# Optimization experiments

Hardware: AMD Instinct MI355X
Metric: run time of the kernel (lower is better)

## Reference

```python
import jax, jax.numpy as jnp
import numpy as np

N_NODES = 10000
N_EDGES = 160000
F_IN, D, DEPTH, F_OUT = 6, 512, 10, 1


def setup_inputs() -> dict:
    key = jax.random.key(0)
    ks = jax.random.split(key, 10)
    features = jax.random.normal(ks[0], (N_NODES, F_IN), dtype=jnp.float32)
    src = jax.random.randint(ks[1], (N_EDGES,), 0, N_NODES, dtype=jnp.int32)
    dst = jax.random.randint(ks[2], (N_EDGES,), 0, N_NODES, dtype=jnp.int32)
    s_in = 1.0 / np.sqrt(F_IN)
    s_h = 1.0 / np.sqrt(D)
    W_in = jax.random.uniform(ks[3], (F_IN, D), jnp.float32, -s_in, s_in)
    b_in = jax.random.uniform(ks[4], (D,), jnp.float32, -s_in, s_in)
    Ws = jax.random.uniform(ks[5], (DEPTH, D, D), jnp.float32, -s_h, s_h)
    bs = jax.random.uniform(ks[6], (DEPTH, D), jnp.float32, -s_h, s_h)
    W_out = jax.random.uniform(ks[7], (D, F_OUT), jnp.float32, -s_h, s_h)
    b_out = jax.random.uniform(ks[8], (F_OUT,), jnp.float32, -s_h, s_h)
    return {"features": features, "W_in": W_in, "b_in": b_in, "Ws": Ws,
            "bs": bs, "W_out": W_out, "b_out": b_out, "src": src, "dst": dst}


def reference(features, W_in, b_in, Ws, bs, W_out, b_out, src, dst):
    n = features.shape[0]
    # GCNLayer: aggregate = scatter-sum of neighbor features (copy_src + sum), then Linear
    agg = jax.ops.segment_sum(features[src], dst, num_segments=n)  # [N, F_in]
    x = jax.nn.relu(agg @ W_in + b_in)  # ReLU only after input layer (per forward)

    def step(x, wb):
        W, b = wb
        a = jax.ops.segment_sum(x[src], dst, num_segments=n)  # [N, D]
        return a @ W + b, None  # no activation between hidden GCN layers

    x, _ = jax.lax.scan(step, x, (Ws, bs))
    return x @ W_out + b_out  # [N, 1]
```

## Files before the change

### kernel.cpp

```cpp
#include <hip/hip_runtime.h>


#define N_NODES 10000
#define N_EDGES 160000
#define DEPTH   10

#define NB_G 40
#define NB_C 33
#define NB   (NB_G + NB_C)
#define BT   1024
#define NTHG (NB_G * BT)
#define NPB  250
#define ECAP 8192

__device__ __forceinline__ float ldA(const float* p) {
    return __hip_atomic_load(p, __ATOMIC_RELAXED, __HIP_MEMORY_SCOPE_AGENT);
}
__device__ __forceinline__ int ldAi(const int* p) {
    return __hip_atomic_load(p, __ATOMIC_RELAXED, __HIP_MEMORY_SCOPE_AGENT);
}
__device__ __forceinline__ void stA(float* p, float v) {
    __hip_atomic_store(p, v, __ATOMIC_RELAXED, __HIP_MEMORY_SCOPE_AGENT);
}
__device__ __forceinline__ void stAi(int* p, int v) {
    __hip_atomic_store(p, v, __ATOMIC_RELAXED, __HIP_MEMORY_SCOPE_AGENT);
}

__device__ __forceinline__ void group_bar(int* flags, int gi, int n, int target) {
    const int tx = threadIdx.x;
    asm volatile("s_waitcnt vmcnt(0)" ::: "memory");
    __syncthreads();
    if (tx == 0) stAi(&flags[gi * 32], target);
    if (tx < n && tx != gi) {
        while (ldAi(&flags[tx * 32]) < target) __builtin_amdgcn_s_sleep(1);
    }
    __syncthreads();
}

extern "C" __global__ void __launch_bounds__(BT, 1) gcn_mega(
    const float* __restrict__ features, const float* __restrict__ W_in,
    const float* __restrict__ b_in, const float* __restrict__ Ws,
    const float* __restrict__ bs, const float* __restrict__ W_out,
    const float* __restrict__ b_out, const int* __restrict__ src,
    const int* __restrict__ dst, float* __restrict__ out,
    int* g_arrive, int* c_arrive, int* rdv, int* deg, int* row_ptr,
    int* cursor, int* esrc, float* vbufs, float* gamma,
    float* rb0, float* rb1)
{
    __shared__ int   lds_e[ECAP];
    __shared__ float s_Wb[4096];
    __shared__ float s_vt[512];
    __shared__ float s_gam[16];
    __shared__ int   s_info[2];
    __shared__ int   s_wsum[16];

    const int tx = threadIdx.x;
    const int bx = blockIdx.x;

    if (bx >= NB_G) {
        const int gi   = bx - NB_G;
        const int cw   = gi * (BT / 64) + (tx >> 6);
        const int lane = tx & 63;
        for (int s = 0; s < DEPTH; s++) {
            const int l = 9 - s;
            if (cw <= 512) {
                float vin[8];
                if (s == 0) {
#pragma unroll
                    for (int c = 0; c < 8; c++) vin[c] = W_out[lane + 64 * c];
                } else {
                    const float* vb = vbufs + (s & 1) * 512;
#pragma unroll
                    for (int c = 0; c < 8; c++) vin[c] = ldA(vb + lane + 64 * c);
                }
                const float* rowp = (cw < 512)
                    ? (Ws + (size_t)l * (512 * 512) + (size_t)cw * 512)
                    : (bs + (size_t)l * 512);
                float acc = 0.f;
#pragma unroll
                for (int c = 0; c < 8; c++) acc += rowp[lane + 64 * c] * vin[c];
#pragma unroll
                for (int off = 32; off; off >>= 1) acc += __shfl_xor(acc, off, 64);
                if (lane == 0) {
                    if (cw < 512) stA(&vbufs[((s + 1) & 1) * 512 + cw], acc);
                    else          stA(&gamma[l], acc);
                }
            }
            if (s < DEPTH - 1) group_bar(c_arrive, gi, NB_C, s + 1);
        }
        asm volatile("s_waitcnt vmcnt(0)" ::: "memory");
        __syncthreads();
        if (tx == 0) stAi(&rdv[gi * 32], 1);
        return;
    }

    const int gi = bx;
    int gt = 1;

    {
        const int t0 = bx * BT + tx;
        for (int e = t0; e < N_EDGES; e += NTHG) atomicAdd(&deg[dst[e]], 1);
    }
    for (int idx = tx; idx < 4096; idx += BT) {
        int j = idx >> 3, k = idx & 7;
        float v = 0.f;
        if (k < 6) v = W_in[k * 512 + j];
        else if (k == 6) v = b_in[j];
        s_Wb[idx] = v;
    }
    group_bar(g_arrive, gi, NB_G, gt++);

    if (bx == 0) {
        const int lane = tx & 63, wid = tx >> 6;
        const bool sact = tx < 1000;
        int lv[10];
        int ssum = 0;
        if (sact) {
#pragma unroll
            for (int i = 0; i < 10; i++) { lv[i] = ldAi(&deg[tx * 10 + i]); ssum += lv[i]; }
        }
        int v = ssum;
#pragma unroll
        for (int off = 1; off < 64; off <<= 1) {
            int u = __shfl_up(v, off, 64);
            if (lane >= off) v += u;
        }
        if (lane == 63) s_wsum[wid] = v;
        __syncthreads();
        if (wid == 0) {
            int w = (lane < 16) ? s_wsum[lane] : 0;
#pragma unroll
            for (int off = 1; off < 16; off <<= 1) {
                int u = __shfl_up(w, off, 64);
                if (lane >= off) w += u;
            }
            if (lane < 16) s_wsum[lane] = w;
        }
        __syncthreads();
        if (sact) {
            int run = (wid ? s_wsum[wid - 1] : 0) + (v - ssum);
#pragma unroll
            for (int i = 0; i < 10; i++) {
                stAi(&row_ptr[tx * 10 + i], run);
                stAi(&cursor[tx * 10 + i], run);
                run += lv[i];
            }
            if (tx == 999) stAi(&row_ptr[N_NODES], run);
        }
    }
    group_bar(g_arrive, gi, NB_G, gt++);

    {
        const int t0 = bx * BT + tx;
        for (int e = t0; e < N_EDGES; e += NTHG) {
            int d = dst[e];
            int sv = src[e];
            int pos = atomicAdd(&cursor[d], 1);
            stAi(&esrc[pos], sv);
        }
    }
    group_bar(g_arrive, gi, NB_G, gt++);

    if (tx == 0) {
        s_info[0] = ldAi(&row_ptr[bx * NPB]);
        s_info[1] = ldAi(&row_ptr[bx * NPB + NPB]);
    }
    __syncthreads();
    const int e_lo = s_info[0];
    const int slen = s_info[1] - e_lo;
    const bool use_lds = (slen <= ECAP);
    if (use_lds) {
        for (int i = tx; i < slen; i += BT) lds_e[i] = ldAi(&esrc[e_lo + i]);
    }
    __syncthreads();

    const int node = bx * NPB + (tx >> 2);
    const int sub  = tx & 3;
    const bool act = tx < 4 * NPB;
    int ns = 0, ne = 0;
    float a0 = 0.f, a1 = 0.f, a2 = 0.f, a3 = 0.f, a4 = 0.f, a5 = 0.f;
    if (act) {
        ns = ldAi(&row_ptr[node]);
        ne = ldAi(&row_ptr[node + 1]);
        if (use_lds) {
            for (int pp = ns + sub; pp < ne; pp += 4) {
                int j = lds_e[pp - e_lo];
                const float2* f = (const float2*)(features + (size_t)j * 6);
                float2 f0 = f[0], f1 = f[1], f2 = f[2];
                a0 += f0.x; a1 += f0.y; a2 += f1.x;
                a3 += f1.y; a4 += f2.x; a5 += f2.y;
            }
        } else {
            for (int pp = ns + sub; pp < ne; pp += 4) {
                int j = ldAi(&esrc[pp]);
                const float2* f = (const float2*)(features + (size_t)j * 6);
                float2 f0 = f[0], f1 = f[1], f2 = f[2];
                a0 += f0.x; a1 += f0.y; a2 += f1.x;
                a3 += f1.y; a4 += f2.x; a5 += f2.y;
            }
        }
        a0 += __shfl_xor(a0, 1, 64); a0 += __shfl_xor(a0, 2, 64);
        a1 += __shfl_xor(a1, 1, 64); a1 += __shfl_xor(a1, 2, 64);
        a2 += __shfl_xor(a2, 1, 64); a2 += __shfl_xor(a2, 2, 64);
        a3 += __shfl_xor(a3, 1, 64); a3 += __shfl_xor(a3, 2, 64);
        a4 += __shfl_xor(a4, 1, 64); a4 += __shfl_xor(a4, 2, 64);
        a5 += __shfl_xor(a5, 1, 64); a5 += __shfl_xor(a5, 2, 64);
    }

    if (tx < NB_C) {
        while (ldAi(&rdv[tx * 32]) < 1) __builtin_amdgcn_s_sleep(1);
    }
    __syncthreads();
    if (tx < 512) s_vt[tx] = ldA(&vbufs[tx]);
    if (tx >= 512 && tx < 512 + DEPTH) s_gam[tx - 512] = ldA(&gamma[tx - 512]);
    __syncthreads();

    if (act) {
        const float4* Wb4 = (const float4*)s_Wb;
        float zacc = 0.f;
#pragma unroll 4
        for (int jj = 0; jj < 128; jj++) {
            int j = (jj << 2) | sub;
            float4 wA = Wb4[2 * j];
            float4 wB = Wb4[2 * j + 1];
            float tv = wB.z + a0 * wA.x + a1 * wA.y + a2 * wA.z +
                       a3 * wA.w + a4 * wB.x + a5 * wB.y;
            zacc += fmaxf(tv, 0.f) * s_vt[j];
        }
        zacc += __shfl_xor(zacc, 1, 64);
        zacc += __shfl_xor(zacc, 2, 64);
        if (sub == 0) stA(&rb0[node], zacc);
    }
    group_bar(g_arrive, gi, NB_G, gt++);

    for (int l = 0; l < DEPTH; l++) {
        if (act) {
            const float* rin = (l & 1) ? rb1 : rb0;
            float h0 = 0.f, h1 = 0.f;
            int pp = ns + sub;
            if (use_lds) {
                for (; pp + 4 < ne; pp += 8) {
                    h0 += ldA(&rin[lds_e[pp - e_lo]]);
                    h1 += ldA(&rin[lds_e[pp + 4 - e_lo]]);
                }
                if (pp < ne) h0 += ldA(&rin[lds_e[pp - e_lo]]);
            } else {
                for (; pp + 4 < ne; pp += 8) {
                    h0 += ldA(&rin[ldAi(&esrc[pp])]);
                    h1 += ldA(&rin[ldAi(&esrc[pp + 4])]);
                }
                if (pp < ne) h0 += ldA(&rin[ldAi(&esrc[pp])]);
            }
            float hs = h0 + h1;
            hs += __shfl_xor(hs, 1, 64);
            hs += __shfl_xor(hs, 2, 64);
            if (sub == 0) {
                float res = hs + s_gam[l];
                if (l == DEPTH - 1) out[node] = res + b_out[0];
                else stA(&((l & 1) ? rb0 : rb1)[node], res);
            }
        }
        if (l < DEPTH - 1) group_bar(g_arrive, gi, NB_G, gt++);
    }
}


extern "C" void kernel_launch(void* const* d_in, const int* in_sizes, int n_in,
                              void* d_out, int out_size, void* d_ws, size_t ws_size,
                              hipStream_t stream) {
    const float* features = (const float*)d_in[0];
    const float* W_in     = (const float*)d_in[1];
    const float* b_in     = (const float*)d_in[2];
    const float* Ws       = (const float*)d_in[3];
    const float* bs       = (const float*)d_in[4];
    const float* W_out    = (const float*)d_in[5];
    const float* b_out    = (const float*)d_in[6];
    const int*   src      = (const int*)d_in[7];
    const int*   dst      = (const int*)d_in[8];
    float* out = (float*)d_out;

    char* base = (char*)d_ws;
    int*   g_arrive = (int*)(base + 0);
    int*   c_arrive = (int*)(base + 5120);
    int*   rdv      = (int*)(base + 10240);
    int*   deg      = (int*)(base + 15360);
    int*   row_ptr  = (int*)(base + 55424);
    int*   cursor   = (int*)(base + 95488);
    int*   esrc     = (int*)(base + 135552);
    float* vbufs    = (float*)(base + 775552);
    float* gamma    = (float*)(base + 779648);
    float* rb0      = (float*)(base + 779712);
    float* rb1      = (float*)(base + 819712);

    hipMemsetAsync(base, 0, 55360, stream);

    gcn_mega<<<NB, BT, 0, stream>>>(features, W_in, b_in, Ws, bs, W_out, b_out,
                                    src, dst, out,
                                    g_arrive, c_arrive, rdv, deg, row_ptr,
                                    cursor, esrc, vbufs, gamma, rb0, rb1);
}
```

Before: 184.0 us.

## Replace grid-group barriers with per-element ready-flag dataflow synchronization

Removes the global group barriers between the edge-sort, scan, chain and per-layer propagation phases. Each produced value is instead stored as a 64-bit word holding the float plus a ready bit, and consumers spin on exactly the elements they read. Per-layer results go to separate slabs, so no double-buffer reuse needs a barrier, and the 4-wide unrolled gather issues independent loads. The cost is a much larger workspace memset, 8-byte traffic for every gathered value, and spin loops on individual elements. The unrolled gather reads lds_e even when the LDS path is disabled, which is only safe while every block's edge range fits in LDS.

```diff
diff --git a/kernel.cpp b/kernel.cpp
--- a/kernel.cpp
+++ b/kernel.cpp
@@ -13,28 +13,34 @@
 #define NPB  250
 #define ECAP 8192
 
-__device__ __forceinline__ float ldA(const float* p) {
-    return __hip_atomic_load(p, __ATOMIC_RELAXED, __HIP_MEMORY_SCOPE_AGENT);
-}
+typedef unsigned long long u64;
+
 __device__ __forceinline__ int ldAi(const int* p) {
     return __hip_atomic_load(p, __ATOMIC_RELAXED, __HIP_MEMORY_SCOPE_AGENT);
 }
-__device__ __forceinline__ void stA(float* p, float v) {
-    __hip_atomic_store(p, v, __ATOMIC_RELAXED, __HIP_MEMORY_SCOPE_AGENT);
-}
 __device__ __forceinline__ void stAi(int* p, int v) {
     __hip_atomic_store(p, v, __ATOMIC_RELAXED, __HIP_MEMORY_SCOPE_AGENT);
 }
-
-__device__ __forceinline__ void group_bar(int* flags, int gi, int n, int target) {
-    const int tx = threadIdx.x;
-    asm volatile("s_waitcnt vmcnt(0)" ::: "memory");
-    __syncthreads();
-    if (tx == 0) stAi(&flags[gi * 32], target);
-    if (tx < n && tx != gi) {
-        while (ldAi(&flags[tx * 32]) < target) __builtin_amdgcn_s_sleep(1);
-    }
-    __syncthreads();
+__device__ __forceinline__ u64 ld8(const u64* p) {
+    return __hip_atomic_load(p, __ATOMIC_RELAXED, __HIP_MEMORY_SCOPE_AGENT);
+}
+__device__ __forceinline__ void st8(u64* p, u64 v) {
+    __hip_atomic_store(p, v, __ATOMIC_RELAXED, __HIP_MEMORY_SCOPE_AGENT);
+}
+__device__ __forceinline__ u64 packf(float f) {
+    union { float f; unsigned u; } c; c.f = f;
+    return (1ull << 32) | (u64)c.u;
+}
+__device__ __forceinline__ float unpackf(u64 v) {
+    union { unsigned u; float f; } c; c.u = (unsigned)v;
+    return c.f;
+}
+#define READY(v) ((unsigned)((v) >> 32) != 0u)
+
+__device__ __forceinline__ float pollf(const u64* p) {
+    u64 v = ld8(p);
+    while (!READY(v)) { __builtin_amdgcn_s_sleep(1); v = ld8(p); }
+    return unpackf(v);
 }
 
 extern "C" __global__ void __launch_bounds__(BT, 1) gcn_mega(
@@ -43,9 +49,8 @@
     const float* __restrict__ bs, const float* __restrict__ W_out,
     const float* __restrict__ b_out, const int* __restrict__ src,
     const int* __restrict__ dst, float* __restrict__ out,
-    int* g_arrive, int* c_arrive, int* rdv, int* deg, int* row_ptr,
-    int* cursor, int* esrc, float* vbufs, float* gamma,
-    float* rb0, float* rb1)
+    int* deg_done, int* scan_done, u64* gamma8, u64* vslab,
+    int* deg, u64* esrc8, u64* rslab, int* row_ptr, int* cursor)
 {
     __shared__ int   lds_e[ECAP];
     __shared__ float s_Wb[4096];
@@ -61,41 +66,48 @@
         const int gi   = bx - NB_G;
         const int cw   = gi * (BT / 64) + (tx >> 6);
         const int lane = tx & 63;
+        if (cw > 512) return;
         for (int s = 0; s < DEPTH; s++) {
             const int l = 9 - s;
-            if (cw <= 512) {
-                float vin[8];
-                if (s == 0) {
-#pragma unroll
-                    for (int c = 0; c < 8; c++) vin[c] = W_out[lane + 64 * c];
-                } else {
-                    const float* vb = vbufs + (s & 1) * 512;
-#pragma unroll
-                    for (int c = 0; c < 8; c++) vin[c] = ldA(vb + lane + 64 * c);
+            const float* rowp = (cw < 512)
+                ? (Ws + (size_t)l * (512 * 512) + (size_t)cw * 512)
+                : (bs + (size_t)l * 512);
+            float wrow[8];
+#pragma unroll
+            for (int c = 0; c < 8; c++) wrow[c] = rowp[lane + 64 * c];
+            float vin[8];
+            if (s == 0) {
+#pragma unroll
+                for (int c = 0; c < 8; c++) vin[c] = W_out[lane + 64 * c];
+            } else {
+                const u64* vb = vslab + (size_t)s * 512;
+                u64 raw[8];
+#pragma unroll
+                for (int c = 0; c < 8; c++) raw[c] = ld8(vb + lane + 64 * c);
+                for (;;) {
+                    bool ok = true;
+#pragma unroll
+                    for (int c = 0; c < 8; c++)
+                        if (!READY(raw[c])) { ok = false; raw[c] = ld8(vb + lane + 64 * c); }
+                    if (ok) break;
+                    __builtin_amdgcn_s_sleep(1);
                 }
-                const float* rowp = (cw < 512)
-                    ? (Ws + (size_t)l * (512 * 512) + (size_t)cw * 512)
-                    : (bs + (size_t)l * 512);
-                float acc = 0.f;
-#pragma unroll
-                for (int c = 0; c < 8; c++) acc += rowp[lane + 64 * c] * vin[c];
-#pragma unroll
-                for (int off = 32; off; off >>= 1) acc += __shfl_xor(acc, off, 64);
-                if (lane == 0) {
-                    if (cw < 512) stA(&vbufs[((s + 1) & 1) * 512 + cw], acc);
-                    else          stA(&gamma[l], acc);
-                }
-            }
-            if (s < DEPTH - 1) group_bar(c_arrive, gi, NB_C, s + 1);
-        }
-        asm volatile("s_waitcnt vmcnt(0)" ::: "memory");
-        __syncthreads();
-        if (tx == 0) stAi(&rdv[gi * 32], 1);
+#pragma unroll
+                for (int c = 0; c < 8; c++) vin[c] = unpackf(raw[c]);
+            }
+            float acc = 0.f;
+#pragma unroll
+            for (int c = 0; c < 8; c++) acc += wrow[c] * vin[c];
+#pragma unroll
+            for (int off = 32; off; off >>= 1) acc += __shfl_xor(acc, off, 64);
+            if (lane == 0) {
+                if (cw < 512) st8(vslab + (size_t)(s + 1) * 512 + cw, packf(acc));
+                else          st8(gamma8 + l, packf(acc));
+            }
+        }
         return;
     }
 
-    const int gi = bx;
-    int gt = 1;
 
     {
         const int t0 = bx * BT + tx;
@@ -108,9 +120,15 @@
         else if (k == 6) v = b_in[j];
         s_Wb[idx] = v;
     }
-    group_bar(g_arrive, gi, NB_G, gt++);
+    asm volatile("s_waitcnt vmcnt(0)" ::: "memory");
+    __syncthreads();
+    if (tx == 0) stAi(&deg_done[bx * 32], 1);
 
     if (bx == 0) {
+        if (tx < NB_G) {
+            while (ldAi(&deg_done[tx * 32]) < 1) __builtin_amdgcn_s_sleep(1);
+        }
+        __syncthreads();
         const int lane = tx & 63, wid = tx >> 6;
         const bool sact = tx < 1000;
         int lv[10];
@@ -147,19 +165,25 @@
             }
             if (tx == 999) stAi(&row_ptr[N_NODES], run);
         }
-    }
-    group_bar(g_arrive, gi, NB_G, gt++);
+        asm volatile("s_waitcnt vmcnt(0)" ::: "memory");
+        __syncthreads();
+        if (tx == 0) stAi(scan_done, 1);
+    } else {
+        if (tx == 0) {
+            while (ldAi(scan_done) < 1) __builtin_amdgcn_s_sleep(1);
+        }
+        __syncthreads();
+    }
 
     {
         const int t0 = bx * BT + tx;
         for (int e = t0; e < N_EDGES; e += NTHG) {
             int d = dst[e];
-            int sv = src[e];
+            unsigned sv = (unsigned)src[e];
             int pos = atomicAdd(&cursor[d], 1);
-            stAi(&esrc[pos], sv);
-        }
-    }
-    group_bar(g_arrive, gi, NB_G, gt++);
+            st8(&esrc8[pos], (1ull << 32) | (u64)sv);
+        }
+    }
 
     if (tx == 0) {
         s_info[0] = ldAi(&row_ptr[bx * NPB]);
@@ -170,7 +194,11 @@
     const int slen = s_info[1] - e_lo;
     const bool use_lds = (slen <= ECAP);
     if (use_lds) {
-        for (int i = tx; i < slen; i += BT) lds_e[i] = ldAi(&esrc[e_lo + i]);
+        for (int i = tx; i < slen; i += BT) {
+            u64 v = ld8(&esrc8[e_lo + i]);
+            while (!READY(v)) { __builtin_amdgcn_s_sleep(1); v = ld8(&esrc8[e_lo + i]); }
+            lds_e[i] = (int)(unsigned)v;
+        }
     }
     __syncthreads();
 
@@ -182,22 +210,18 @@
     if (act) {
         ns = ldAi(&row_ptr[node]);
         ne = ldAi(&row_ptr[node + 1]);
-        if (use_lds) {
-            for (int pp = ns + sub; pp < ne; pp += 4) {
-                int j = lds_e[pp - e_lo];
-                const float2* f = (const float2*)(features + (size_t)j * 6);
-                float2 f0 = f[0], f1 = f[1], f2 = f[2];
-                a0 += f0.x; a1 += f0.y; a2 += f1.x;
-                a3 += f1.y; a4 += f2.x; a5 += f2.y;
-            }
-        } else {
-            for (int pp = ns + sub; pp < ne; pp += 4) {
-                int j = ldAi(&esrc[pp]);
-                const float2* f = (const float2*)(features + (size_t)j * 6);
-                float2 f0 = f[0], f1 = f[1], f2 = f[2];
-                a0 += f0.x; a1 += f0.y; a2 += f1.x;
-                a3 += f1.y; a4 += f2.x; a5 += f2.y;
-            }
+        for (int pp = ns + sub; pp < ne; pp += 4) {
+            int j;
+            if (use_lds) j = lds_e[pp - e_lo];
+            else {
+                u64 v = ld8(&esrc8[pp]);
+                while (!READY(v)) { __builtin_amdgcn_s_sleep(1); v = ld8(&esrc8[pp]); }
+                j = (int)(unsigned)v;
+            }
+            const float2* f = (const float2*)(features + (size_t)j * 6);
+            float2 f0 = f[0], f1 = f[1], f2 = f[2];
+            a0 += f0.x; a1 += f0.y; a2 += f1.x;
+            a3 += f1.y; a4 += f2.x; a5 += f2.y;
         }
         a0 += __shfl_xor(a0, 1, 64); a0 += __shfl_xor(a0, 2, 64);
         a1 += __shfl_xor(a1, 1, 64); a1 += __shfl_xor(a1, 2, 64);
@@ -207,12 +231,8 @@
         a5 += __shfl_xor(a5, 1, 64); a5 += __shfl_xor(a5, 2, 64);
     }
 
-    if (tx < NB_C) {
-        while (ldAi(&rdv[tx * 32]) < 1) __builtin_amdgcn_s_sleep(1);
-    }
-    __syncthreads();
-    if (tx < 512) s_vt[tx] = ldA(&vbufs[tx]);
-    if (tx >= 512 && tx < 512 + DEPTH) s_gam[tx - 512] = ldA(&gamma[tx - 512]);
+    if (tx < 512) s_vt[tx] = pollf(vslab + 10 * 512 + tx);
+    else if (tx < 512 + DEPTH) s_gam[tx - 512] = pollf(gamma8 + (tx - 512));
     __syncthreads();
 
     if (act) {
@@ -229,40 +249,50 @@
         }
         zacc += __shfl_xor(zacc, 1, 64);
         zacc += __shfl_xor(zacc, 2, 64);
-        if (sub == 0) stA(&rb0[node], zacc);
-    }
-    group_bar(g_arrive, gi, NB_G, gt++);
+        if (sub == 0) st8(&rslab[node], packf(zacc));
+    }
 
     for (int l = 0; l < DEPTH; l++) {
         if (act) {
-            const float* rin = (l & 1) ? rb1 : rb0;
-            float h0 = 0.f, h1 = 0.f;
+            const u64* rin = rslab + (size_t)l * N_NODES;
+            float h = 0.f;
             int pp = ns + sub;
-            if (use_lds) {
-                for (; pp + 4 < ne; pp += 8) {
-                    h0 += ldA(&rin[lds_e[pp - e_lo]]);
-                    h1 += ldA(&rin[lds_e[pp + 4 - e_lo]]);
+            for (; pp + 12 < ne; pp += 16) {
+                int i0 = lds_e[pp - e_lo],     i1 = lds_e[pp + 4 - e_lo];
+                int i2 = lds_e[pp + 8 - e_lo], i3 = lds_e[pp + 12 - e_lo];
+                u64 v0 = ld8(rin + i0), v1 = ld8(rin + i1);
+                u64 v2 = ld8(rin + i2), v3 = ld8(rin + i3);
+                while (!(READY(v0) && READY(v1) && READY(v2) && READY(v3))) {
+                    if (!READY(v0)) v0 = ld8(rin + i0);
+                    if (!READY(v1)) v1 = ld8(rin + i1);
+                    if (!READY(v2)) v2 = ld8(rin + i2);
+                    if (!READY(v3)) v3 = ld8(rin + i3);
                 }
-                if (pp < ne) h0 += ldA(&rin[lds_e[pp - e_lo]]);
-            } else {
-                for (; pp + 4 < ne; pp += 8) {
-                    h0 += ldA(&rin[ldAi(&esrc[pp])]);
-                    h1 += ldA(&rin[ldAi(&esrc[pp + 4])]);
+                h += unpackf(v0) + unpackf(v1) + unpackf(v2) + unpackf(v3);
+            }
+            for (; pp < ne; pp += 4) {
+                int j;
+                if (use_lds) j = lds_e[pp - e_lo];
+                else {
+                    u64 ev = ld8(&esrc8[pp]);
+                    while (!READY(ev)) { __builtin_amdgcn_s_sleep(1); ev = ld8(&esrc8[pp]); }
+                    j = (int)(unsigned)ev;
                 }
-                if (pp < ne) h0 += ldA(&rin[ldAi(&esrc[pp])]);
-            }
-            float hs = h0 + h1;
-            hs += __shfl_xor(hs, 1, 64);
-            hs += __shfl_xor(hs, 2, 64);
+                u64 v = ld8(rin + j);
+                while (!READY(v)) v = ld8(rin + j);
+                h += unpackf(v);
+            }
+            h += __shfl_xor(h, 1, 64);
+            h += __shfl_xor(h, 2, 64);
             if (sub == 0) {
-                float res = hs + s_gam[l];
+                float res = h + s_gam[l];
                 if (l == DEPTH - 1) out[node] = res + b_out[0];
-                else stA(&((l & 1) ? rb0 : rb1)[node], res);
-            }
-        }
-        if (l < DEPTH - 1) group_bar(g_arrive, gi, NB_G, gt++);
-    }
-}
+                else st8(&rslab[(size_t)(l + 1) * N_NODES + node], packf(res));
+            }
+        }
+    }
+}
+
 
 
 extern "C" void kernel_launch(void* const* d_in, const int* in_sizes, int n_in,
@@ -280,22 +310,21 @@
     float* out = (float*)d_out;
 
     char* base = (char*)d_ws;
-    int*   g_arrive = (int*)(base + 0);
-    int*   c_arrive = (int*)(base + 5120);
-    int*   rdv      = (int*)(base + 10240);
-    int*   deg      = (int*)(base + 15360);
-    int*   row_ptr  = (int*)(base + 55424);
-    int*   cursor   = (int*)(base + 95488);
-    int*   esrc     = (int*)(base + 135552);
-    float* vbufs    = (float*)(base + 775552);
-    float* gamma    = (float*)(base + 779648);
-    float* rb0      = (float*)(base + 779712);
-    float* rb1      = (float*)(base + 819712);
-
-    hipMemsetAsync(base, 0, 55360, stream);
+    int* deg_done  = (int*)(base + 0);
+    int* scan_done = (int*)(base + 5120);
+    u64* gamma8    = (u64*)(base + 5248);
+    u64* vslab     = (u64*)(base + 5376);
+    int* deg       = (int*)(base + 50432);
+    u64* esrc8     = (u64*)(base + 90432);
+    u64* rslab     = (u64*)(base + 1370432);
+    const size_t MEMSET_END = 2250432;
+    int* row_ptr   = (int*)(base + 2250432);
+    int* cursor    = (int*)(base + 2290560);
+
+    hipMemsetAsync(base, 0, MEMSET_END, stream);
 
     gcn_mega<<<NB, BT, 0, stream>>>(features, W_in, b_in, Ws, bs, W_out, b_out,
                                     src, dst, out,
-                                    g_arrive, c_arrive, rdv, deg, row_ptr,
-                                    cursor, esrc, vbufs, gamma, rb0, rb1);
-}
+                                    deg_done, scan_done, gamma8, vslab,
+                                    deg, esrc8, rslab, row_ptr, cursor);
+}
```

New measurement: 249.6 us. 1.36x slower.
